# Performance work log

Measured on AMD Instinct MI355X. Metric: run time of the kernel, lower is better.

The kernel has to match this reference:

```python
import jax, jax.numpy as jnp
import numpy as np

E, W, C, N, Q = 8, 5, 640, 49, 75


def setup_inputs() -> dict:
    key = jax.random.key(0)
    k1, k2 = jax.random.split(key)
    proto = jax.random.normal(k1, (E, W, C, 1, N), dtype=jnp.float32)
    query = jax.random.normal(k2, (E, Q, C, 1, N), dtype=jnp.float32)
    return {"proto": proto, "query": query}


def reference(proto, query):
    # proto: [E, W, C, 1, N] -> [E, W, C, N]; query: [E, Q, C, 1, N] -> [E, Q, C, N]
    p = jnp.squeeze(proto, axis=3)
    q = jnp.squeeze(query, axis=3)
    # cosine similarity map over channel dim C:
    # sim[e,q,w,n,m] = <p[e,w,:,n], q[e,q,:,m]>
    sim = jnp.einsum('ewcn,eqcm->eqwnm', p, q)
    norm_p = jnp.linalg.norm(p, axis=2)  # [E, W, N]
    norm_q = jnp.linalg.norm(q, axis=2)  # [E, Q, N]
    denom = norm_p[:, None, :, :, None] * norm_q[:, :, None, None, :] + 1e-8
    return sim / denom  # [E, Q, W, N, N]
```

## Files before the change

kernel.cpp:

```cpp
#include <hip/hip_runtime.h>
#include <hip/hip_bf16.h>


#define E_CNT 8
#define W_CNT 5
#define C_CNT 640
#define N_CNT 49
#define Q_CNT 75
#define MROWS 245
#define NC32 20
#define AFRAG_CH 16384
#define AIMG_E (NC32 * AFRAG_CH)
#define AIMG_SIZE (E_CNT * AIMG_E)
#define PN_OFF AIMG_SIZE
#define PN_BYTES (E_CNT * 10 * MROWS * 4)
#define WS1 ((size_t)(PN_OFF + PN_BYTES))

typedef __attribute__((ext_vector_type(8))) short bf16x8;
typedef __attribute__((ext_vector_type(4))) float f32x4;

static __device__ __forceinline__ short f2bf(float f) {
    __hip_bfloat16 h = __float2bfloat16(f);
    return *reinterpret_cast<short*>(&h);
}

#define RAW_BARRIER() asm volatile("s_waitcnt lgkmcnt(0)\n\ts_barrier" ::: "memory")

__global__ __launch_bounds__(256, 4)
void prep_a_kernel(const float* __restrict__ proto,
                   unsigned char* __restrict__ aimg,
                   float* __restrict__ pn_part)
{
    __shared__ float pns[MROWS];
    const int b = blockIdx.x;
    const int e = b / 10, c64 = b % 10;
    const float* pbase = proto + (size_t)e * (W_CNT * C_CNT * N_CNT);
    unsigned char* ebase = aimg + (size_t)e * AIMG_E;
    const int t = threadIdx.x;
    if (t < MROWS) pns[t] = 0.f;
    __syncthreads();

    #pragma unroll
    for (int i = 0; i < 8; ++i) {
        const int s = t + i * 256;
        int nw, kb;
        bf16x8 pk;
        if (s < 8 * MROWS) {
            kb = s / MROWS;
            nw = s - kb * MROWS;
            const int w = nw / N_CNT, n = nw - w * N_CNT;
            const float* g = pbase + ((size_t)(w * C_CNT + c64 * 64 + kb * 8)) * N_CNT + n;
            float ss = 0.f;
            #pragma unroll
            for (int j = 0; j < 8; ++j) {
                const float f = g[(size_t)j * N_CNT];
                ss += f * f;
                pk[j] = f2bf(f);
            }
            atomicAdd(&pns[nw], ss);
        } else {
            const int x = s - 8 * MROWS;
            nw = MROWS + (x >> 3);
            kb = x & 7;
            pk = (bf16x8){0, 0, 0, 0, 0, 0, 0, 0};
        }
        const int c32 = c64 * 2 + (kb >> 2);
        const int ln2 = ((kb & 3) << 4) | (nw & 15);
        *reinterpret_cast<bf16x8*>(
            ebase + (size_t)c32 * AFRAG_CH + (size_t)((nw >> 4) * 64 + ln2) * 16) = pk;
    }
    __syncthreads();
    if (t < MROWS) pn_part[(size_t)(e * 10 + c64) * MROWS + t] = pns[t];
}

__global__ __launch_bounds__(512, 4)
void gemm9_kernel(const float* __restrict__ query,
                  const unsigned char* __restrict__ aimg,
                  const float* __restrict__ pn_part,
                  float* __restrict__ out)
{
    __shared__ __align__(16) unsigned char Bbuf[2 * 4096];
    __shared__ float qn[64];
    __shared__ float pnl[256];

    const int b = blockIdx.x;
    const int e = b & 7;
    const int q = b >> 3;
    const int eq = e * Q_CNT + q;
    const int t = threadIdx.x;
    const int wv = t >> 6, ln = t & 63;
    const int lrow = ln & 15, lk = ln >> 4;

    const float* __restrict__ qsl = query + (size_t)eq * (C_CNT * N_CNT);

    const bool stg = t < 256;
    const int fjS = (t >> 6) & 3;
    const int lnS = t & 63;
    const int scol = fjS * 16 + (t & 15);
    const int scolc = (scol < N_CNT) ? scol : (N_CNT - 1);
    const int lkS = (t >> 4) & 3;
    const float* __restrict__ sbase = qsl + (size_t)(lkS * 8) * N_CNT + scolc;
    const int swoff = fjS * 1024 + lnS * 16;

    const unsigned char* __restrict__ abase =
        aimg + (size_t)e * AIMG_E + (size_t)((wv * 2) * 64 + ln) * 16;

    if (t < MROWS) {
        float s = 0.f;
        #pragma unroll
        for (int cc = 0; cc < 10; ++cc)
            s += pn_part[(size_t)(e * 10 + cc) * MROWS + t];
        pnl[t] = sqrtf(s);
    }

    float vBA0, vBA1, vBA2, vBA3, vBA4, vBA5, vBA6, vBA7;
    float vBB0, vBB1, vBB2, vBB3, vBB4, vBB5, vBB6, vBB7;
    bf16x8 afrA0, afrA1, afrB0, afrB1;
    f32x4 acc[2][4];
    #pragma unroll
    for (int i = 0; i < 2; ++i)
        #pragma unroll
        for (int j = 0; j < 4; ++j) acc[i][j] = (f32x4){0.f, 0.f, 0.f, 0.f};
    float ssq = 0.f;

#define BISSUE_A(c) do { if (stg) {                                             \
    const size_t k0_ = (size_t)(c) * 32 * N_CNT;                                \
    vBA0 = sbase[k0_];              vBA1 = sbase[k0_ + 1 * N_CNT];              \
    vBA2 = sbase[k0_ + 2 * N_CNT];  vBA3 = sbase[k0_ + 3 * N_CNT];              \
    vBA4 = sbase[k0_ + 4 * N_CNT];  vBA5 = sbase[k0_ + 5 * N_CNT];              \
    vBA6 = sbase[k0_ + 6 * N_CNT];  vBA7 = sbase[k0_ + 7 * N_CNT]; } } while (0)

#define BISSUE_B(c) do { if (stg) {                                             \
    const size_t k0_ = (size_t)(c) * 32 * N_CNT;                                \
    vBB0 = sbase[k0_];              vBB1 = sbase[k0_ + 1 * N_CNT];              \
    vBB2 = sbase[k0_ + 2 * N_CNT];  vBB3 = sbase[k0_ + 3 * N_CNT];              \
    vBB4 = sbase[k0_ + 4 * N_CNT];  vBB5 = sbase[k0_ + 5 * N_CNT];              \
    vBB6 = sbase[k0_ + 6 * N_CNT];  vBB7 = sbase[k0_ + 7 * N_CNT]; } } while (0)

#define CVTW_A(bufofs) do { if (stg) {                                          \
    bf16x8 pk_;                                                                 \
    ssq += vBA0*vBA0 + vBA1*vBA1 + vBA2*vBA2 + vBA3*vBA3                        \
         + vBA4*vBA4 + vBA5*vBA5 + vBA6*vBA6 + vBA7*vBA7;                       \
    pk_[0]=f2bf(vBA0); pk_[1]=f2bf(vBA1); pk_[2]=f2bf(vBA2); pk_[3]=f2bf(vBA3); \
    pk_[4]=f2bf(vBA4); pk_[5]=f2bf(vBA5); pk_[6]=f2bf(vBA6); pk_[7]=f2bf(vBA7); \
    *reinterpret_cast<bf16x8*>(Bbuf + (bufofs) + swoff) = pk_; } } while (0)

#define CVTW_B(bufofs) do { if (stg) {                                          \
    bf16x8 pk_;                                                                 \
    ssq += vBB0*vBB0 + vBB1*vBB1 + vBB2*vBB2 + vBB3*vBB3                        \
         + vBB4*vBB4 + vBB5*vBB5 + vBB6*vBB6 + vBB7*vBB7;                       \
    pk_[0]=f2bf(vBB0); pk_[1]=f2bf(vBB1); pk_[2]=f2bf(vBB2); pk_[3]=f2bf(vBB3); \
    pk_[4]=f2bf(vBB4); pk_[5]=f2bf(vBB5); pk_[6]=f2bf(vBB6); pk_[7]=f2bf(vBB7); \
    *reinterpret_cast<bf16x8*>(Bbuf + (bufofs) + swoff) = pk_; } } while (0)

#define AISSUE_A(c) do {                                                        \
    afrA0 = *reinterpret_cast<const bf16x8*>(abase + (size_t)(c) * AFRAG_CH);   \
    afrA1 = *reinterpret_cast<const bf16x8*>(abase + (size_t)(c) * AFRAG_CH + 1024); \
} while (0)

#define AISSUE_B(c) do {                                                        \
    afrB0 = *reinterpret_cast<const bf16x8*>(abase + (size_t)(c) * AFRAG_CH);   \
    afrB1 = *reinterpret_cast<const bf16x8*>(abase + (size_t)(c) * AFRAG_CH + 1024); \
} while (0)

#define DO_MFMA(a0, a1, bufofs) do {                                            \
    bf16x8 bfr0_ = *reinterpret_cast<const bf16x8*>(Bbuf + (bufofs) + 0 * 1024 + ln * 16); \
    bf16x8 bfr1_ = *reinterpret_cast<const bf16x8*>(Bbuf + (bufofs) + 1 * 1024 + ln * 16); \
    bf16x8 bfr2_ = *reinterpret_cast<const bf16x8*>(Bbuf + (bufofs) + 2 * 1024 + ln * 16); \
    bf16x8 bfr3_ = *reinterpret_cast<const bf16x8*>(Bbuf + (bufofs) + 3 * 1024 + ln * 16); \
    acc[0][0] = __builtin_amdgcn_mfma_f32_16x16x32_bf16(a0, bfr0_, acc[0][0], 0, 0, 0); \
    acc[0][1] = __builtin_amdgcn_mfma_f32_16x16x32_bf16(a0, bfr1_, acc[0][1], 0, 0, 0); \
    acc[0][2] = __builtin_amdgcn_mfma_f32_16x16x32_bf16(a0, bfr2_, acc[0][2], 0, 0, 0); \
    acc[0][3] = __builtin_amdgcn_mfma_f32_16x16x32_bf16(a0, bfr3_, acc[0][3], 0, 0, 0); \
    acc[1][0] = __builtin_amdgcn_mfma_f32_16x16x32_bf16(a1, bfr0_, acc[1][0], 0, 0, 0); \
    acc[1][1] = __builtin_amdgcn_mfma_f32_16x16x32_bf16(a1, bfr1_, acc[1][1], 0, 0, 0); \
    acc[1][2] = __builtin_amdgcn_mfma_f32_16x16x32_bf16(a1, bfr2_, acc[1][2], 0, 0, 0); \
    acc[1][3] = __builtin_amdgcn_mfma_f32_16x16x32_bf16(a1, bfr3_, acc[1][3], 0, 0, 0); \
} while (0)

    BISSUE_A(0);
    AISSUE_A(0);
    BISSUE_B(1);
    CVTW_A(0);
    RAW_BARRIER();

    for (int cc = 0; cc < NC32; cc += 2) {
        const bool lastpair = (cc == NC32 - 2);
        if (!lastpair) BISSUE_A(cc + 2);
        AISSUE_B(cc + 1);
        DO_MFMA(afrA0, afrA1, 0);
        CVTW_B(4096);
        RAW_BARRIER();
        if (!lastpair) {
            BISSUE_B(cc + 3);
            AISSUE_A(cc + 2);
        }
        DO_MFMA(afrB0, afrB1, 4096);
        if (!lastpair) {
            CVTW_A(0);
            RAW_BARRIER();
        }
    }

    {
        float s = ssq;
        s += __shfl_xor(s, 16);
        s += __shfl_xor(s, 32);
        if (stg && lkS == 0) qn[fjS * 16 + (t & 15)] = s;
    }
    __syncthreads();

    float nq4[4];
    #pragma unroll
    for (int fj = 0; fj < 4; ++fj) {
        const int m = fj * 16 + lrow;
        nq4[fj] = (m < N_CNT) ? sqrtf(qn[m]) : 1.f;
    }
    float* __restrict__ osl = out + (size_t)eq * (W_CNT * N_CNT * N_CNT);
    #pragma unroll
    for (int fi = 0; fi < 2; ++fi) {
        #pragma unroll
        for (int rr = 0; rr < 4; ++rr) {
            const int row = wv * 32 + fi * 16 + lk * 4 + rr;
            if (row < MROWS) {
                const float np_ = pnl[row];
                #pragma unroll
                for (int fj = 0; fj < 4; ++fj) {
                    const int m = fj * 16 + lrow;
                    if (m < N_CNT) {
                        const float den = np_ * nq4[fj] + 1e-8f;
                        osl[row * N_CNT + m] = acc[fi][fj][rr] * __builtin_amdgcn_rcpf(den);
                    }
                }
            }
        }
    }
#undef BISSUE_A
#undef BISSUE_B
#undef CVTW_A
#undef CVTW_B
#undef AISSUE_A
#undef AISSUE_B
#undef DO_MFMA
}

struct SMemFB {
    unsigned char A[256 * 128];
    unsigned char B[64 * 128];
    float ns[320];
};

__global__ __launch_bounds__(512, 4)
void sim_fallback_kernel(const float* __restrict__ proto,
                         const float* __restrict__ query,
                         float* __restrict__ out)
{
    __shared__ SMemFB smf;
    const int t = threadIdx.x;
    const int e = blockIdx.x / Q_CNT;
    const int q = blockIdx.x - e * Q_CNT;
    const float* pbase = proto + (size_t)e * (W_CNT * C_CNT * N_CNT);
    const float* qbase = query + ((size_t)e * Q_CNT + q) * (C_CNT * N_CNT);
    unsigned char* lds = (unsigned char*)&smf;
    if (t < 320) smf.ns[t] = 0.f;
    if (t < 208) {
        if (t < 88) *reinterpret_cast<f32x4*>(smf.A + 245 * 128 + t * 16) = (f32x4){0.f,0.f,0.f,0.f};
        else        *reinterpret_cast<f32x4*>(smf.B + 49 * 128 + (t - 88) * 16) = (f32x4){0.f,0.f,0.f,0.f};
    }
    const int nslot5 = (t < 304);
    const float* gp[5];
    int offidx[5];
    #pragma unroll
    for (int i = 0; i < 5; ++i) {
        gp[i] = pbase; offidx[i] = 0;
        if (i < 4 || nslot5) {
            const int s = t + i * 512;
            if (s < 1960) {
                const int kb = s / 245, nw = s - kb * 245;
                const int w = nw / 49, n = nw - w * 49;
                gp[i] = pbase + ((size_t)w * C_CNT + kb * 8) * N_CNT + n;
                offidx[i] = (nw * 128 + ((kb ^ (nw & 7)) << 4)) | (nw << 16);
            } else {
                const int s2 = s - 1960;
                const int kb = s2 / 49, mq = s2 - kb * 49;
                gp[i] = qbase + (size_t)(kb * 8) * N_CNT + mq;
                offidx[i] = (32768 + mq * 128 + ((kb ^ (mq & 7)) << 4)) | ((256 + mq) << 16);
            }
        }
    }
    float v[5][8];
    float ss[5] = {0.f,0.f,0.f,0.f,0.f};
    #pragma unroll
    for (int i = 0; i < 4; ++i)
        #pragma unroll
        for (int j = 0; j < 8; ++j) v[i][j] = gp[i][(size_t)j * N_CNT];
    if (nslot5)
        #pragma unroll
        for (int j = 0; j < 8; ++j) v[4][j] = gp[4][(size_t)j * N_CNT];
    f32x4 acc[2][4];
    #pragma unroll
    for (int i = 0; i < 2; ++i)
        #pragma unroll
        for (int j = 0; j < 4; ++j) acc[i][j] = (f32x4){0.f,0.f,0.f,0.f};
    const int wv = t >> 6, ln = t & 63, lrow = ln & 15, lk = ln >> 4;
    for (int kc = 0; kc < 10; ++kc) {
        #pragma unroll
        for (int i = 0; i < 5; ++i) {
            if (i < 4 || nslot5) {
                bf16x8 pk; float s8 = 0.f;
                #pragma unroll
                for (int j = 0; j < 8; ++j) { const float f = v[i][j]; s8 += f*f; pk[j] = f2bf(f); }
                ss[i] += s8;
                *reinterpret_cast<bf16x8*>(lds + (offidx[i] & 0xFFFF)) = pk;
            }
        }
        __syncthreads();
        if (kc < 9) {
            #pragma unroll
            for (int i = 0; i < 4; ++i) {
                gp[i] += 64 * N_CNT;
                #pragma unroll
                for (int j = 0; j < 8; ++j) v[i][j] = gp[i][(size_t)j * N_CNT];
            }
            if (nslot5) {
                gp[4] += 64 * N_CNT;
                #pragma unroll
                for (int j = 0; j < 8; ++j) v[4][j] = gp[4][(size_t)j * N_CNT];
            }
        }
        #pragma unroll
        for (int ks = 0; ks < 2; ++ks) {
            bf16x8 af[2], bfr[4];
            #pragma unroll
            for (int i = 0; i < 2; ++i) {
                const int row = (wv * 2 + i) * 16 + lrow;
                const int gr = (ks * 4 + lk) ^ (row & 7);
                af[i] = *reinterpret_cast<const bf16x8*>(lds + row * 128 + gr * 16);
            }
            #pragma unroll
            for (int j = 0; j < 4; ++j) {
                const int mq = j * 16 + lrow;
                const int gr = (ks * 4 + lk) ^ (mq & 7);
                bfr[j] = *reinterpret_cast<const bf16x8*>(lds + 32768 + mq * 128 + gr * 16);
            }
            #pragma unroll
            for (int i = 0; i < 2; ++i)
                #pragma unroll
                for (int j = 0; j < 4; ++j)
                    acc[i][j] = __builtin_amdgcn_mfma_f32_16x16x32_bf16(af[i], bfr[j], acc[i][j], 0, 0, 0);
        }
        __syncthreads();
    }
    #pragma unroll
    for (int i = 0; i < 5; ++i)
        if (i < 4 || nslot5) atomicAdd(&smf.ns[offidx[i] >> 16], ss[i]);
    __syncthreads();
    float nq[4];
    #pragma unroll
    for (int j = 0; j < 4; ++j) {
        const int mq = j * 16 + lrow;
        nq[j] = (mq < N_CNT) ? sqrtf(smf.ns[256 + mq]) : 1.f;
    }
    float* obase = out + (size_t)(e * Q_CNT + q) * (W_CNT * N_CNT * N_CNT);
    #pragma unroll
    for (int i = 0; i < 2; ++i) {
        #pragma unroll
        for (int rr = 0; rr < 4; ++rr) {
            const int nw = (wv * 2 + i) * 16 + lk * 4 + rr;
            if (nw < W_CNT * N_CNT) {
                const int w = nw / 49, n = nw - w * 49;
                const float np_ = sqrtf(smf.ns[nw]);
                float* orow = obase + ((size_t)w * N_CNT + n) * N_CNT;
                #pragma unroll
                for (int j = 0; j < 4; ++j) {
                    const int mq = j * 16 + lrow;
                    if (mq < N_CNT) orow[mq] = acc[i][j][rr] / (np_ * nq[j] + 1e-8f);
                }
            }
        }
    }
}

extern "C" void kernel_launch(void* const* d_in, const int* in_sizes, int n_in,
                              void* d_out, int out_size, void* d_ws, size_t ws_size,
                              hipStream_t stream)
{
    const float* proto = (const float*)d_in[0];
    const float* query = (const float*)d_in[1];
    float* out = (float*)d_out;

    if (ws_size < WS1) {
        hipLaunchKernelGGL(sim_fallback_kernel, dim3(E_CNT * Q_CNT), dim3(512), 0, stream,
                           proto, query, out);
        return;
    }

    unsigned char* aimg = (unsigned char*)d_ws;
    float* pn_part = (float*)((unsigned char*)d_ws + PN_OFF);

    hipLaunchKernelGGL(prep_a_kernel, dim3(E_CNT * 10), dim3(256), 0, stream,
                       proto, aimg, pn_part);
    hipLaunchKernelGGL(gemm9_kernel, dim3(E_CNT * Q_CNT), dim3(512), 0, stream,
                       query, aimg, pn_part, out);
}
```

Measured before the change: 42.94 us.

## Stage whole query slice into LDS upfront, then run barrier-free MFMA loop

The GEMM kernel now converts the entire query slice (all 20 K-chunks) to bf16 in an 80KB LDS buffer before any MFMA work. All 512 threads take part in staging instead of 256, and the query norms are accumulated with LDS atomics. The main loop then runs with no per-chunk barriers, removing the double-buffer handshake. The cost is far more LDS per block (launch bounds drop to 2 blocks per CU) and losing the overlap between global loads and MFMA inside a block.

```diff
diff --git a/kernel.cpp b/kernel.cpp
--- a/kernel.cpp
+++ b/kernel.cpp
@@ -23,8 +23,6 @@
     __hip_bfloat16 h = __float2bfloat16(f);
     return *reinterpret_cast<short*>(&h);
 }
-
-#define RAW_BARRIER() asm volatile("s_waitcnt lgkmcnt(0)\n\ts_barrier" ::: "memory")
 
 __global__ __launch_bounds__(256, 4)
 void prep_a_kernel(const float* __restrict__ proto,
@@ -73,13 +71,13 @@
     if (t < MROWS) pn_part[(size_t)(e * 10 + c64) * MROWS + t] = pns[t];
 }
 
-__global__ __launch_bounds__(512, 4)
-void gemm9_kernel(const float* __restrict__ query,
-                  const unsigned char* __restrict__ aimg,
-                  const float* __restrict__ pn_part,
-                  float* __restrict__ out)
+__global__ __launch_bounds__(512, 2)
+void gemm10_kernel(const float* __restrict__ query,
+                   const unsigned char* __restrict__ aimg,
+                   const float* __restrict__ pn_part,
+                   float* __restrict__ out)
 {
-    __shared__ __align__(16) unsigned char Bbuf[2 * 4096];
+    __shared__ __align__(16) unsigned char Ball[NC32 * 4096];
     __shared__ float qn[64];
     __shared__ float pnl[256];
 
@@ -93,18 +91,20 @@
 
     const float* __restrict__ qsl = query + (size_t)eq * (C_CNT * N_CNT);
 
-    const bool stg = t < 256;
-    const int fjS = (t >> 6) & 3;
-    const int lnS = t & 63;
-    const int scol = fjS * 16 + (t & 15);
-    const int scolc = (scol < N_CNT) ? scol : (N_CNT - 1);
-    const int lkS = (t >> 4) & 3;
-    const float* __restrict__ sbase = qsl + (size_t)(lkS * 8) * N_CNT + scolc;
+    const int slot = t & 255;
+    const int par  = t >> 8;
+    const int fjS  = slot >> 6;
+    const int lnS  = slot & 63;
+    const int col  = fjS * 16 + (slot & 15);
+    const int colc = (col < N_CNT) ? col : (N_CNT - 1);
+    const int lkS  = (slot >> 4) & 3;
+    const float* __restrict__ sbase = qsl + (size_t)(lkS * 8) * N_CNT + colc;
     const int swoff = fjS * 1024 + lnS * 16;
 
     const unsigned char* __restrict__ abase =
         aimg + (size_t)e * AIMG_E + (size_t)((wv * 2) * 64 + ln) * 16;
 
+    if (t < 64) qn[t] = 0.f;
     if (t < MROWS) {
         float s = 0.f;
         #pragma unroll
@@ -112,46 +112,76 @@
             s += pn_part[(size_t)(e * 10 + cc) * MROWS + t];
         pnl[t] = sqrtf(s);
     }
-
-    float vBA0, vBA1, vBA2, vBA3, vBA4, vBA5, vBA6, vBA7;
-    float vBB0, vBB1, vBB2, vBB3, vBB4, vBB5, vBB6, vBB7;
+    __syncthreads();
+
+    float sA0, sA1, sA2, sA3, sA4, sA5, sA6, sA7;
+    float sB0, sB1, sB2, sB3, sB4, sB5, sB6, sB7;
+    float ssq = 0.f;
+
+#define SLOAD_A(c) do {                                                         \
+    const float* p_ = sbase + (size_t)((c) * 32) * N_CNT;                       \
+    sA0 = p_[0];          sA1 = p_[1 * N_CNT];                                  \
+    sA2 = p_[2 * N_CNT];  sA3 = p_[3 * N_CNT];                                  \
+    sA4 = p_[4 * N_CNT];  sA5 = p_[5 * N_CNT];                                  \
+    sA6 = p_[6 * N_CNT];  sA7 = p_[7 * N_CNT];                                  \
+} while (0)
+
+#define SLOAD_B(c) do {                                                         \
+    const float* p_ = sbase + (size_t)((c) * 32) * N_CNT;                       \
+    sB0 = p_[0];          sB1 = p_[1 * N_CNT];                                  \
+    sB2 = p_[2 * N_CNT];  sB3 = p_[3 * N_CNT];                                  \
+    sB4 = p_[4 * N_CNT];  sB5 = p_[5 * N_CNT];                                  \
+    sB6 = p_[6 * N_CNT];  sB7 = p_[7 * N_CNT];                                  \
+} while (0)
+
+#define SPROC_A(c) do {                                                         \
+    bf16x8 pk_;                                                                 \
+    ssq += sA0*sA0 + sA1*sA1 + sA2*sA2 + sA3*sA3                                \
+         + sA4*sA4 + sA5*sA5 + sA6*sA6 + sA7*sA7;                               \
+    pk_[0]=f2bf(sA0); pk_[1]=f2bf(sA1); pk_[2]=f2bf(sA2); pk_[3]=f2bf(sA3);     \
+    pk_[4]=f2bf(sA4); pk_[5]=f2bf(sA5); pk_[6]=f2bf(sA6); pk_[7]=f2bf(sA7);     \
+    *reinterpret_cast<bf16x8*>(Ball + (c) * 4096 + swoff) = pk_;                \
+} while (0)
+
+#define SPROC_B(c) do {                                                         \
+    bf16x8 pk_;                                                                 \
+    ssq += sB0*sB0 + sB1*sB1 + sB2*sB2 + sB3*sB3                                \
+         + sB4*sB4 + sB5*sB5 + sB6*sB6 + sB7*sB7;                               \
+    pk_[0]=f2bf(sB0); pk_[1]=f2bf(sB1); pk_[2]=f2bf(sB2); pk_[3]=f2bf(sB3);     \
+    pk_[4]=f2bf(sB4); pk_[5]=f2bf(sB5); pk_[6]=f2bf(sB6); pk_[7]=f2bf(sB7);     \
+    *reinterpret_cast<bf16x8*>(Ball + (c) * 4096 + swoff) = pk_;                \
+} while (0)
+
+    SLOAD_A(par);
+    SLOAD_B(par + 2);
+    SPROC_A(par);
+    SLOAD_A(par + 4);
+    SPROC_B(par + 2);
+    SLOAD_B(par + 6);
+    SPROC_A(par + 4);
+    SLOAD_A(par + 8);
+    SPROC_B(par + 6);
+    SLOAD_B(par + 10);
+    SPROC_A(par + 8);
+    SLOAD_A(par + 12);
+    SPROC_B(par + 10);
+    SLOAD_B(par + 14);
+    SPROC_A(par + 12);
+    SLOAD_A(par + 16);
+    SPROC_B(par + 14);
+    SLOAD_B(par + 18);
+    SPROC_A(par + 16);
+    SPROC_B(par + 18);
+
+    atomicAdd(&qn[col], ssq);
+    __syncthreads();
+
     bf16x8 afrA0, afrA1, afrB0, afrB1;
     f32x4 acc[2][4];
     #pragma unroll
     for (int i = 0; i < 2; ++i)
         #pragma unroll
         for (int j = 0; j < 4; ++j) acc[i][j] = (f32x4){0.f, 0.f, 0.f, 0.f};
-    float ssq = 0.f;
-
-#define BISSUE_A(c) do { if (stg) {                                             \
-    const size_t k0_ = (size_t)(c) * 32 * N_CNT;                                \
-    vBA0 = sbase[k0_];              vBA1 = sbase[k0_ + 1 * N_CNT];              \
-    vBA2 = sbase[k0_ + 2 * N_CNT];  vBA3 = sbase[k0_ + 3 * N_CNT];              \
-    vBA4 = sbase[k0_ + 4 * N_CNT];  vBA5 = sbase[k0_ + 5 * N_CNT];              \
-    vBA6 = sbase[k0_ + 6 * N_CNT];  vBA7 = sbase[k0_ + 7 * N_CNT]; } } while (0)
-
-#define BISSUE_B(c) do { if (stg) {                                             \
-    const size_t k0_ = (size_t)(c) * 32 * N_CNT;                                \
-    vBB0 = sbase[k0_];              vBB1 = sbase[k0_ + 1 * N_CNT];              \
-    vBB2 = sbase[k0_ + 2 * N_CNT];  vBB3 = sbase[k0_ + 3 * N_CNT];              \
-    vBB4 = sbase[k0_ + 4 * N_CNT];  vBB5 = sbase[k0_ + 5 * N_CNT];              \
-    vBB6 = sbase[k0_ + 6 * N_CNT];  vBB7 = sbase[k0_ + 7 * N_CNT]; } } while (0)
-
-#define CVTW_A(bufofs) do { if (stg) {                                          \
-    bf16x8 pk_;                                                                 \
-    ssq += vBA0*vBA0 + vBA1*vBA1 + vBA2*vBA2 + vBA3*vBA3                        \
-         + vBA4*vBA4 + vBA5*vBA5 + vBA6*vBA6 + vBA7*vBA7;                       \
-    pk_[0]=f2bf(vBA0); pk_[1]=f2bf(vBA1); pk_[2]=f2bf(vBA2); pk_[3]=f2bf(vBA3); \
-    pk_[4]=f2bf(vBA4); pk_[5]=f2bf(vBA5); pk_[6]=f2bf(vBA6); pk_[7]=f2bf(vBA7); \
-    *reinterpret_cast<bf16x8*>(Bbuf + (bufofs) + swoff) = pk_; } } while (0)
-
-#define CVTW_B(bufofs) do { if (stg) {                                          \
-    bf16x8 pk_;                                                                 \
-    ssq += vBB0*vBB0 + vBB1*vBB1 + vBB2*vBB2 + vBB3*vBB3                        \
-         + vBB4*vBB4 + vBB5*vBB5 + vBB6*vBB6 + vBB7*vBB7;                       \
-    pk_[0]=f2bf(vBB0); pk_[1]=f2bf(vBB1); pk_[2]=f2bf(vBB2); pk_[3]=f2bf(vBB3); \
-    pk_[4]=f2bf(vBB4); pk_[5]=f2bf(vBB5); pk_[6]=f2bf(vBB6); pk_[7]=f2bf(vBB7); \
-    *reinterpret_cast<bf16x8*>(Bbuf + (bufofs) + swoff) = pk_; } } while (0)
 
 #define AISSUE_A(c) do {                                                        \
     afrA0 = *reinterpret_cast<const bf16x8*>(abase + (size_t)(c) * AFRAG_CH);   \
@@ -163,11 +193,12 @@
     afrB1 = *reinterpret_cast<const bf16x8*>(abase + (size_t)(c) * AFRAG_CH + 1024); \
 } while (0)
 
-#define DO_MFMA(a0, a1, bufofs) do {                                            \
-    bf16x8 bfr0_ = *reinterpret_cast<const bf16x8*>(Bbuf + (bufofs) + 0 * 1024 + ln * 16); \
-    bf16x8 bfr1_ = *reinterpret_cast<const bf16x8*>(Bbuf + (bufofs) + 1 * 1024 + ln * 16); \
-    bf16x8 bfr2_ = *reinterpret_cast<const bf16x8*>(Bbuf + (bufofs) + 2 * 1024 + ln * 16); \
-    bf16x8 bfr3_ = *reinterpret_cast<const bf16x8*>(Bbuf + (bufofs) + 3 * 1024 + ln * 16); \
+#define DO_MFMA(c, a0, a1) do {                                                 \
+    const unsigned char* bb_ = Ball + (c) * 4096;                               \
+    bf16x8 bfr0_ = *reinterpret_cast<const bf16x8*>(bb_ + 0 * 1024 + ln * 16);  \
+    bf16x8 bfr1_ = *reinterpret_cast<const bf16x8*>(bb_ + 1 * 1024 + ln * 16);  \
+    bf16x8 bfr2_ = *reinterpret_cast<const bf16x8*>(bb_ + 2 * 1024 + ln * 16);  \
+    bf16x8 bfr3_ = *reinterpret_cast<const bf16x8*>(bb_ + 3 * 1024 + ln * 16);  \
     acc[0][0] = __builtin_amdgcn_mfma_f32_16x16x32_bf16(a0, bfr0_, acc[0][0], 0, 0, 0); \
     acc[0][1] = __builtin_amdgcn_mfma_f32_16x16x32_bf16(a0, bfr1_, acc[0][1], 0, 0, 0); \
     acc[0][2] = __builtin_amdgcn_mfma_f32_16x16x32_bf16(a0, bfr2_, acc[0][2], 0, 0, 0); \
@@ -178,37 +209,13 @@
     acc[1][3] = __builtin_amdgcn_mfma_f32_16x16x32_bf16(a1, bfr3_, acc[1][3], 0, 0, 0); \
 } while (0)
 
-    BISSUE_A(0);
     AISSUE_A(0);
-    BISSUE_B(1);
-    CVTW_A(0);
-    RAW_BARRIER();
-
     for (int cc = 0; cc < NC32; cc += 2) {
-        const bool lastpair = (cc == NC32 - 2);
-        if (!lastpair) BISSUE_A(cc + 2);
         AISSUE_B(cc + 1);
-        DO_MFMA(afrA0, afrA1, 0);
-        CVTW_B(4096);
-        RAW_BARRIER();
-        if (!lastpair) {
-            BISSUE_B(cc + 3);
-            AISSUE_A(cc + 2);
-        }
-        DO_MFMA(afrB0, afrB1, 4096);
-        if (!lastpair) {
-            CVTW_A(0);
-            RAW_BARRIER();
-        }
-    }
-
-    {
-        float s = ssq;
-        s += __shfl_xor(s, 16);
-        s += __shfl_xor(s, 32);
-        if (stg && lkS == 0) qn[fjS * 16 + (t & 15)] = s;
-    }
-    __syncthreads();
+        DO_MFMA(cc, afrA0, afrA1);
+        if (cc + 2 < NC32) AISSUE_A(cc + 2);
+        DO_MFMA(cc + 1, afrB0, afrB1);
+    }
 
     float nq4[4];
     #pragma unroll
@@ -235,10 +242,10 @@
             }
         }
     }
-#undef BISSUE_A
-#undef BISSUE_B
-#undef CVTW_A
-#undef CVTW_B
+#undef SLOAD_A
+#undef SLOAD_B
+#undef SPROC_A
+#undef SPROC_B
 #undef AISSUE_A
 #undef AISSUE_B
 #undef DO_MFMA
@@ -400,6 +407,6 @@
 
     hipLaunchKernelGGL(prep_a_kernel, dim3(E_CNT * 10), dim3(256), 0, stream,
                        proto, aimg, pn_part);
-    hipLaunchKernelGGL(gemm9_kernel, dim3(E_CNT * Q_CNT), dim3(512), 0, stream,
+    hipLaunchKernelGGL(gemm10_kernel, dim3(E_CNT * Q_CNT), dim3(512), 0, stream,
                        query, aimg, pn_part, out);
 }
```

New measurement: 52.76 us. 22.9% more time.
